# Kernel tuning notes

Measured on AMD Instinct MI355X. Metric: run time of the kernel, lower is better.

## Reference

```python
import jax, jax.numpy as jnp
import numpy as np

RES = 32
HEADS = 16
EMB = 1024
DIM_HEAD = EMB // HEADS
BATCH = 8
N = RES * RES
SCALE = DIM_HEAD ** -0.5


def _make_bias_idxs():
    # replicate the LeViT-style |dx|,|dy| offset indexing from __init__
    points = [(i, j) for i in range(RES) for j in range(RES)]
    offsets = {}
    idxs = []
    for p1 in points:
        for p2 in points:
            off = (abs(p1[0] - p2[0]), abs(p1[1] - p2[1]))
            if off not in offsets:
                offsets[off] = len(offsets)
            idxs.append(offsets[off])
    return np.asarray(idxs, dtype=np.int32).reshape(N, N), len(offsets)


def setup_inputs() -> dict:
    key = jax.random.key(0)
    k_x, k_qkv, k_b, k_o = jax.random.split(key, 4)
    bias_idxs, n_off = _make_bias_idxs()  # n_off == 1024 for a 32x32 grid
    return {
        "x": jax.random.normal(k_x, (BATCH, N, EMB), dtype=jnp.float32),
        "W_qkv": jax.random.normal(k_qkv, (3 * EMB, EMB), dtype=jnp.float32) * 0.02,
        "attention_biases": jax.random.normal(k_b, (HEADS, n_off), dtype=jnp.float32) * 0.02,
        "bias_idxs": jnp.asarray(bias_idxs),
        "W_out": jax.random.normal(k_o, (EMB, EMB), dtype=jnp.float32) * 0.02,
        "b_out": jnp.zeros((EMB,), dtype=jnp.float32),
    }


def reference(x, W_qkv, attention_biases, bias_idxs, W_out, b_out):
    B, n, E = x.shape
    # to_qkv: Linear(E, 3E, bias=False) -> x @ W^T
    qkv = x @ W_qkv.T  # [B, n, 3E]
    q, k, v = jnp.split(qkv, 3, axis=-1)

    def heads(t):  # b n (h d) -> b h n d
        return t.reshape(B, n, HEADS, DIM_HEAD).transpose(0, 2, 1, 3)

    q, k, v = heads(q), heads(k), heads(v)
    qk = jnp.einsum("bhnd,bhmd->bhnm", q, k) * SCALE  # [B, h, n, n]
    bias = attention_biases[:, bias_idxs]  # gather -> [h, n, n]
    qk = qk + bias[None]
    attn = jax.nn.softmax(qk, axis=-1)
    out = jnp.einsum("bhnm,bhmd->bhnd", attn, v)
    out = out.transpose(0, 2, 1, 3).reshape(B, n, E)  # b h n d -> b n (h d)
    # to_out: Linear(E, E) with bias (dropout p=0 is identity)
    return out @ W_out.T + b_out
```

## Files before the change

### kernel.cpp

```cpp
#include <hip/hip_runtime.h>

typedef __attribute__((ext_vector_type(8))) short bf16x8;
typedef __attribute__((ext_vector_type(4))) short bf16x4;
typedef __attribute__((ext_vector_type(4))) float f32x4;

#define L2E 1.44269504088896340736f
#define QSCL 0.18033688011112042f

__device__ inline unsigned short f2bf(float f) {
  union { float f; unsigned int u; } x; x.f = f;
  return (unsigned short)((x.u + 0x8000u) >> 16);
}
__device__ inline unsigned int f2bf2(float a, float b) {
  union { float f; unsigned int u; } xa, xb;
  xa.f = a; xb.f = b;
  return ((xa.u + 0x8000u) >> 16) | (((xb.u + 0x8000u) & 0xFFFF0000u));
}

__device__ inline void gl_lds16(const void* g, void* l) {
  __builtin_amdgcn_global_load_lds((const __attribute__((address_space(1))) void*)g,
                                   (__attribute__((address_space(3))) void*)l,
                                   16, 0, 0);
}

__global__ void cast_bf16_kernel(const float* __restrict__ in,
                                 unsigned short* __restrict__ out, int n4) {
  int i = blockIdx.x * blockDim.x + threadIdx.x;
  int st = gridDim.x * blockDim.x;
  for (; i < n4; i += st) {
    float4 v = reinterpret_cast<const float4*>(in)[i];
    ushort4 o;
    o.x = f2bf(v.x); o.y = f2bf(v.y); o.z = f2bf(v.z); o.w = f2bf(v.w);
    reinterpret_cast<ushort4*>(out)[i] = o;
  }
}

__global__ __launch_bounds__(256, 2) void gemm_qkv(
    const unsigned short* __restrict__ A,
    const unsigned short* __restrict__ Bm,
    unsigned short* __restrict__ qo,
    unsigned short* __restrict__ ko,
    unsigned short* __restrict__ vo) {
  __shared__ unsigned short sA[2][128 * 32];
  __shared__ unsigned short sB[2][128 * 32];
  __shared__ unsigned short sT[128 * 136];
  const int K = 1024;
  const int tid = threadIdx.x;
  const int w = tid >> 6, lane = tid & 63;
  const int l15 = lane & 15, quad = lane >> 4;
  const int wm = (w >> 1) * 64, wn = (w & 1) * 64;
  const int tm = blockIdx.y, tn = blockIdx.x;

  const unsigned short* Ab = A + (size_t)(tm * 128) * K;
  const unsigned short* Bb = Bm + (size_t)(tn * 128) * K;

  const int srow = w * 32 + (lane >> 2);
  const int scol = (lane & 3) * 8;

  const f32x4 fz = {0.f, 0.f, 0.f, 0.f};
  f32x4 acc[4][4];
#pragma unroll
  for (int i = 0; i < 4; i++)
#pragma unroll
    for (int j = 0; j < 4; j++) acc[i][j] = fz;

  gl_lds16(Ab + (size_t)srow * K + scol,        &sA[0][(w * 32) * 32]);
  gl_lds16(Ab + (size_t)(srow + 16) * K + scol, &sA[0][(w * 32 + 16) * 32]);
  gl_lds16(Bb + (size_t)srow * K + scol,        &sB[0][(w * 32) * 32]);
  gl_lds16(Bb + (size_t)(srow + 16) * K + scol, &sB[0][(w * 32 + 16) * 32]);

  int buf = 0;
  for (int k0 = 0; k0 < K; k0 += 32) {
    __syncthreads();
    if (k0 + 32 < K) {
      int nb = buf ^ 1, kn = k0 + 32;
      gl_lds16(Ab + (size_t)srow * K + kn + scol,        &sA[nb][(w * 32) * 32]);
      gl_lds16(Ab + (size_t)(srow + 16) * K + kn + scol, &sA[nb][(w * 32 + 16) * 32]);
      gl_lds16(Bb + (size_t)srow * K + kn + scol,        &sB[nb][(w * 32) * 32]);
      gl_lds16(Bb + (size_t)(srow + 16) * K + kn + scol, &sB[nb][(w * 32 + 16) * 32]);
    }
    bf16x8 af[4], bfr[4];
#pragma unroll
    for (int mt = 0; mt < 4; mt++) af[mt]  = *(const bf16x8*)&sA[buf][(wm + mt * 16 + l15) * 32 + quad * 8];
#pragma unroll
    for (int nt = 0; nt < 4; nt++) bfr[nt] = *(const bf16x8*)&sB[buf][(wn + nt * 16 + l15) * 32 + quad * 8];
#pragma unroll
    for (int mt = 0; mt < 4; mt++)
#pragma unroll
      for (int nt = 0; nt < 4; nt++)
        acc[mt][nt] = __builtin_amdgcn_mfma_f32_16x16x32_bf16(af[mt], bfr[nt], acc[mt][nt], 0, 0, 0);
    buf ^= 1;
  }

  const int c0 = tn * 128;
  const int which = c0 >> 10;
  const int m0 = tm * 128;
  const int bb = m0 >> 10, n0 = m0 & 1023;
  __syncthreads();
  if (which < 2) {
    const float scl = (which == 0) ? QSCL : 1.0f;
#pragma unroll
    for (int mt = 0; mt < 4; mt++)
#pragma unroll
      for (int nt = 0; nt < 4; nt++)
#pragma unroll
        for (int r = 0; r < 4; r++)
          sT[(wm + mt * 16 + quad * 4 + r) * 136 + wn + nt * 16 + l15] = f2bf(acc[mt][nt][r] * scl);
    __syncthreads();
    unsigned short* dst = (which == 0) ? qo : ko;
#pragma unroll
    for (int i = 0; i < 8; i++) {
      int u = tid + i * 256;
      int row = u >> 4, g = u & 15;
      int cg = c0 + g * 8;
      int hh = (cg & 1023) >> 6, d0 = cg & 63;
      uint4 val = *(const uint4*)&sT[row * 136 + g * 8];
      *(uint4*)&dst[(((size_t)bb * 16 + hh) * 1024 + n0 + row) * 64 + d0] = val;
    }
  } else {
#pragma unroll
    for (int mt = 0; mt < 4; mt++)
#pragma unroll
      for (int nt = 0; nt < 4; nt++)
#pragma unroll
        for (int r = 0; r < 4; r++)
          sT[(wn + nt * 16 + l15) * 136 + wm + mt * 16 + quad * 4 + r] = f2bf(acc[mt][nt][r]);
    __syncthreads();
#pragma unroll
    for (int i = 0; i < 8; i++) {
      int u = tid + i * 256;
      int col = u >> 4, g = u & 15;
      int cg = c0 + col;
      int hh = (cg & 1023) >> 6, dd = cg & 63;
      uint4 val = *(const uint4*)&sT[col * 136 + g * 8];
      *(uint4*)&vo[(((size_t)bb * 16 + hh) * 64 + dd) * 1024 + n0 + g * 8] = val;
    }
  }
}

__global__ __launch_bounds__(256, 4) void attn_kernel(
    const unsigned short* __restrict__ Q,
    const unsigned short* __restrict__ Kg,
    const unsigned short* __restrict__ Vt,
    const float* __restrict__ biases,
    unsigned short* __restrict__ Og) {
  __shared__ unsigned short sK[2][64 * 64];
  __shared__ unsigned short sV[2][64 * 64];
  __shared__ float sBias[1024];

  const int bx = blockIdx.x;
  const int bh = bx & 127, qt = bx >> 7;
  const int h = bh & 15, b = bh >> 4;
  const int tid = threadIdx.x, w = tid >> 6, lane = tid & 63;
  const int l15 = lane & 15, quad = lane >> 4;

  const size_t bhs = (size_t)(b * 16 + h);
  const unsigned short* qbase = Q + (bhs * 1024 + (size_t)qt * 128) * 64;
  const unsigned short* kbase = Kg + bhs * 1024 * 64;
  const unsigned short* vbase = Vt + bhs * 64 * 1024;

  for (int t = tid; t < 1024; t += 256) sBias[t] = biases[h * 1024 + t] * L2E;

  const int sr0 = w * 16 + (lane >> 3);
  const int sc8 = lane & 7;
  const int sw0 = sc8 ^ (lane >> 3);

  gl_lds16(kbase + (size_t)sr0 * 64 + sw0 * 8,        &sK[0][(w * 16) * 64]);
  gl_lds16(kbase + (size_t)(sr0 + 8) * 64 + sw0 * 8,  &sK[0][(w * 16 + 8) * 64]);
  gl_lds16(vbase + (size_t)sr0 * 1024 + sw0 * 8,      &sV[0][(w * 16) * 64]);
  gl_lds16(vbase + (size_t)(sr0 + 8) * 1024 + sw0 * 8,&sV[0][(w * 16 + 8) * 64]);

  bf16x8 qf[2][2];
#pragma unroll
  for (int qb = 0; qb < 2; qb++)
#pragma unroll
    for (int kd = 0; kd < 2; kd++)
      qf[qb][kd] = *(const bf16x8*)(qbase + (w * 32 + qb * 16 + l15) * 64 + kd * 32 + quad * 8);

  const int qg0 = qt * 128 + w * 32;
  int qi[2], qj[2];
#pragma unroll
  for (int qb = 0; qb < 2; qb++) {
    int qr = qg0 + qb * 16 + l15;
    qi[qb] = qr >> 5; qj[qb] = qr & 31;
  }
  const int kvq = quad * 4;

  float rsum[2] = {0.f, 0.f};
  const f32x4 fz = {0.f, 0.f, 0.f, 0.f};
  f32x4 of[2][4];
#pragma unroll
  for (int i = 0; i < 2; i++)
#pragma unroll
    for (int j = 0; j < 4; j++) of[i][j] = fz;

  int buf = 0;
  for (int j0 = 0; j0 < 1024; j0 += 64) {
    __syncthreads();
    if (j0 + 64 < 1024) {
      int nb = buf ^ 1, jn = j0 + 64;
      gl_lds16(kbase + (size_t)(jn + sr0) * 64 + sw0 * 8,       &sK[nb][(w * 16) * 64]);
      gl_lds16(kbase + (size_t)(jn + sr0 + 8) * 64 + sw0 * 8,   &sK[nb][(w * 16 + 8) * 64]);
      gl_lds16(vbase + (size_t)sr0 * 1024 + jn + sw0 * 8,       &sV[nb][(w * 16) * 64]);
      gl_lds16(vbase + (size_t)(sr0 + 8) * 1024 + jn + sw0 * 8, &sV[nb][(w * 16 + 8) * 64]);
    }
    const unsigned short* K_ = sK[buf];
    const unsigned short* V_ = sV[buf];
    const int j5 = j0 >> 5;

#pragma unroll
    for (int kvb = 0; kvb < 4; kvb++) {
      bf16x8 kf0 = *(const bf16x8*)&K_[(kvb * 16 + l15) * 64 + ((quad ^ (l15 & 7)) << 3)];
      bf16x8 kf1 = *(const bf16x8*)&K_[(kvb * 16 + l15) * 64 + (((4 + quad) ^ (l15 & 7)) << 3)];
      bf16x4 vf[4];
#pragma unroll
      for (int nt = 0; nt < 4; nt++) {
        int d = nt * 16 + l15;
        vf[nt] = *(const bf16x4*)&V_[d * 64 + (((kvb * 2 + (quad >> 1)) ^ (l15 & 7)) << 3) + (quad & 1) * 4];
      }
      const int kvi = j5 + (kvb >> 1);
      const int kvjb = (kvb & 1) * 16 + kvq;
#pragma unroll
      for (int qb = 0; qb < 2; qb++) {
        f32x4 s4 = __builtin_amdgcn_mfma_f32_16x16x32_bf16(kf0, qf[qb][0], fz, 0, 0, 0);
        s4 = __builtin_amdgcn_mfma_f32_16x16x32_bf16(kf1, qf[qb][1], s4, 0, 0, 0);
        const float* bb = sBias + (abs(qi[qb] - kvi) << 5);
        float p0 = __builtin_amdgcn_exp2f(s4.x + bb[abs(qj[qb] - kvjb)]);
        float p1 = __builtin_amdgcn_exp2f(s4.y + bb[abs(qj[qb] - (kvjb + 1))]);
        float p2 = __builtin_amdgcn_exp2f(s4.z + bb[abs(qj[qb] - (kvjb + 2))]);
        float p3 = __builtin_amdgcn_exp2f(s4.w + bb[abs(qj[qb] - (kvjb + 3))]);
        rsum[qb] += (p0 + p1) + (p2 + p3);
        union { unsigned int u[2]; bf16x4 v; } pk;
        pk.u[0] = f2bf2(p0, p1);
        pk.u[1] = f2bf2(p2, p3);
#pragma unroll
        for (int nt = 0; nt < 4; nt++)
          of[qb][nt] = __builtin_amdgcn_mfma_f32_16x16x16bf16_1k(pk.v, vf[nt], of[qb][nt], 0, 0, 0);
      }
    }
    buf ^= 1;
  }

#pragma unroll
  for (int qb = 0; qb < 2; qb++) {
    rsum[qb] += __shfl_xor(rsum[qb], 16);
    rsum[qb] += __shfl_xor(rsum[qb], 32);
  }

#pragma unroll
  for (int qb = 0; qb < 2; qb++)
#pragma unroll
    for (int r = 0; r < 4; r++) {
      float rv = __shfl(rsum[qb], kvq + r, 16);
      float inv = __builtin_amdgcn_rcpf(rv);
      int n = qg0 + qb * 16 + kvq + r;
      size_t orow = ((size_t)b * 1024 + n) * 1024 + h * 64;
#pragma unroll
      for (int nt = 0; nt < 4; nt++)
        Og[orow + nt * 16 + l15] = f2bf(of[qb][nt][r] * inv);
    }
}

__global__ __launch_bounds__(256, 2) void gemm_out_k(
    const unsigned short* __restrict__ A,
    const unsigned short* __restrict__ Bm,
    const float* __restrict__ bias,
    float* __restrict__ out) {
  __shared__ unsigned short sA[2][128 * 32];
  __shared__ unsigned short sB[2][128 * 32];
  const int K = 1024;
  const int tid = threadIdx.x;
  const int w = tid >> 6, lane = tid & 63;
  const int l15 = lane & 15, quad = lane >> 4;
  const int wm = (w >> 1) * 64, wn = (w & 1) * 64;
  const int tm = blockIdx.y, tn = blockIdx.x;

  const unsigned short* Ab = A + (size_t)(tm * 128) * K;
  const unsigned short* Bb = Bm + (size_t)(tn * 128) * K;

  const int srow = w * 32 + (lane >> 2);
  const int scol = (lane & 3) * 8;

  const f32x4 fz = {0.f, 0.f, 0.f, 0.f};
  f32x4 acc[4][4];
#pragma unroll
  for (int i = 0; i < 4; i++)
#pragma unroll
    for (int j = 0; j < 4; j++) acc[i][j] = fz;

  gl_lds16(Ab + (size_t)srow * K + scol,        &sA[0][(w * 32) * 32]);
  gl_lds16(Ab + (size_t)(srow + 16) * K + scol, &sA[0][(w * 32 + 16) * 32]);
  gl_lds16(Bb + (size_t)srow * K + scol,        &sB[0][(w * 32) * 32]);
  gl_lds16(Bb + (size_t)(srow + 16) * K + scol, &sB[0][(w * 32 + 16) * 32]);

  int buf = 0;
  for (int k0 = 0; k0 < K; k0 += 32) {
    __syncthreads();
    if (k0 + 32 < K) {
      int nb = buf ^ 1, kn = k0 + 32;
      gl_lds16(Ab + (size_t)srow * K + kn + scol,        &sA[nb][(w * 32) * 32]);
      gl_lds16(Ab + (size_t)(srow + 16) * K + kn + scol, &sA[nb][(w * 32 + 16) * 32]);
      gl_lds16(Bb + (size_t)srow * K + kn + scol,        &sB[nb][(w * 32) * 32]);
      gl_lds16(Bb + (size_t)(srow + 16) * K + kn + scol, &sB[nb][(w * 32 + 16) * 32]);
    }
    bf16x8 af[4], bfr[4];
#pragma unroll
    for (int mt = 0; mt < 4; mt++) af[mt]  = *(const bf16x8*)&sA[buf][(wm + mt * 16 + l15) * 32 + quad * 8];
#pragma unroll
    for (int nt = 0; nt < 4; nt++) bfr[nt] = *(const bf16x8*)&sB[buf][(wn + nt * 16 + l15) * 32 + quad * 8];
#pragma unroll
    for (int mt = 0; mt < 4; mt++)
#pragma unroll
      for (int nt = 0; nt < 4; nt++)
        acc[mt][nt] = __builtin_amdgcn_mfma_f32_16x16x32_bf16(af[mt], bfr[nt], acc[mt][nt], 0, 0, 0);
    buf ^= 1;
  }

  const int m0 = tm * 128 + wm, c0 = tn * 128 + wn;
#pragma unroll
  for (int mt = 0; mt < 4; mt++)
#pragma unroll
    for (int nt = 0; nt < 4; nt++)
#pragma unroll
      for (int r = 0; r < 4; r++) {
        int m = m0 + mt * 16 + quad * 4 + r;
        int c = c0 + nt * 16 + l15;
        out[(size_t)m * 1024 + c] = acc[mt][nt][r] + bias[c];
      }
}

extern "C" void kernel_launch(void* const* d_in, const int* in_sizes, int n_in,
                              void* d_out, int out_size, void* d_ws, size_t ws_size,
                              hipStream_t stream) {
  const float* x    = (const float*)d_in[0];
  const float* Wqkv = (const float*)d_in[1];
  const float* ab   = (const float*)d_in[2];
  const float* Wout = (const float*)d_in[4];
  const float* bout = (const float*)d_in[5];
  float* out = (float*)d_out;

  char* ws = (char*)d_ws;
  unsigned short* xb  = (unsigned short*)(ws);
  unsigned short* wqb = (unsigned short*)(ws + 16777216);
  unsigned short* wob = (unsigned short*)(ws + 23068672);
  unsigned short* qw  = (unsigned short*)(ws + 25165824);
  unsigned short* kw  = (unsigned short*)(ws + 41943040);
  unsigned short* vw  = (unsigned short*)(ws + 58720256);
  unsigned short* ow  = (unsigned short*)(ws + 75497472);

  cast_bf16_kernel<<<1024, 256, 0, stream>>>(x, xb, 8192 * 1024 / 4);
  cast_bf16_kernel<<<512, 256, 0, stream>>>(Wqkv, wqb, 3072 * 1024 / 4);
  cast_bf16_kernel<<<256, 256, 0, stream>>>(Wout, wob, 1024 * 1024 / 4);
  gemm_qkv<<<dim3(24, 64), 256, 0, stream>>>(xb, wqb, qw, kw, vw);
  attn_kernel<<<1024, 256, 0, stream>>>(qw, kw, vw, ab, ow);
  gemm_out_k<<<dim3(8, 64), 256, 0, stream>>>(ow, wob, bout, out);
}
```

Baseline: 264.9 us.

## Swizzle GEMM LDS tiles, drop epilogue staging, split QKV GEMM by output mode

Applies an XOR swizzle to the LDS layout of the A/B tiles in both GEMMs to reduce bank conflicts. The QKV GEMM epilogue no longer stages through a shared transpose buffer. Operand order in the MFMA is swapped for Q/K, and V is written directly, so each lane stores 8-byte packed bf16 values. The QKV GEMM is split into two template launches (Q/K and V), and launch bounds are raised to 4 blocks per SM for more occupancy. Explicit vmcnt(0) waits are added before the barriers so async global->LDS loads have landed. The risk is narrower uncoalesced stores and a second kernel launch.

```diff
diff --git a/kernel.cpp b/kernel.cpp
--- a/kernel.cpp
+++ b/kernel.cpp
@@ -21,6 +21,10 @@
   __builtin_amdgcn_global_load_lds((const __attribute__((address_space(1))) void*)g,
                                    (__attribute__((address_space(3))) void*)l,
                                    16, 0, 0);
+}
+
+__device__ inline void vm_drain() {
+  asm volatile("s_waitcnt vmcnt(0)" ::: "memory");
 }
 
 __global__ void cast_bf16_kernel(const float* __restrict__ in,
@@ -35,7 +39,8 @@
   }
 }
 
-__global__ __launch_bounds__(256, 2) void gemm_qkv(
+template <int MODE>
+__global__ __launch_bounds__(256, 4) void gemm_qkv_t(
     const unsigned short* __restrict__ A,
     const unsigned short* __restrict__ Bm,
     unsigned short* __restrict__ qo,
@@ -43,19 +48,20 @@
     unsigned short* __restrict__ vo) {
   __shared__ unsigned short sA[2][128 * 32];
   __shared__ unsigned short sB[2][128 * 32];
-  __shared__ unsigned short sT[128 * 136];
   const int K = 1024;
   const int tid = threadIdx.x;
   const int w = tid >> 6, lane = tid & 63;
   const int l15 = lane & 15, quad = lane >> 4;
   const int wm = (w >> 1) * 64, wn = (w & 1) * 64;
-  const int tm = blockIdx.y, tn = blockIdx.x;
+  const int tm = blockIdx.y;
+  const int tn = (MODE == 0) ? blockIdx.x : blockIdx.x + 16;
 
   const unsigned short* Ab = A + (size_t)(tm * 128) * K;
   const unsigned short* Bb = Bm + (size_t)(tn * 128) * K;
 
   const int srow = w * 32 + (lane >> 2);
-  const int scol = (lane & 3) * 8;
+  const int scol = (((lane & 3) ^ ((lane >> 3) & 3))) * 8;
+  const int rsw = (l15 >> 1) & 3;
 
   const f32x4 fz = {0.f, 0.f, 0.f, 0.f};
   f32x4 acc[4][4];
@@ -71,6 +77,7 @@
 
   int buf = 0;
   for (int k0 = 0; k0 < K; k0 += 32) {
+    vm_drain();
     __syncthreads();
     if (k0 + 32 < K) {
       int nb = buf ^ 1, kn = k0 + 32;
@@ -81,59 +88,57 @@
     }
     bf16x8 af[4], bfr[4];
 #pragma unroll
-    for (int mt = 0; mt < 4; mt++) af[mt]  = *(const bf16x8*)&sA[buf][(wm + mt * 16 + l15) * 32 + quad * 8];
-#pragma unroll
-    for (int nt = 0; nt < 4; nt++) bfr[nt] = *(const bf16x8*)&sB[buf][(wn + nt * 16 + l15) * 32 + quad * 8];
-#pragma unroll
     for (int mt = 0; mt < 4; mt++)
-#pragma unroll
-      for (int nt = 0; nt < 4; nt++)
-        acc[mt][nt] = __builtin_amdgcn_mfma_f32_16x16x32_bf16(af[mt], bfr[nt], acc[mt][nt], 0, 0, 0);
+      af[mt] = *(const bf16x8*)&sA[buf][(wm + mt * 16 + l15) * 32 + ((quad ^ rsw) << 3)];
+#pragma unroll
+    for (int nt = 0; nt < 4; nt++)
+      bfr[nt] = *(const bf16x8*)&sB[buf][(wn + nt * 16 + l15) * 32 + ((quad ^ rsw) << 3)];
+#pragma unroll
+    for (int mt = 0; mt < 4; mt++)
+#pragma unroll
+      for (int nt = 0; nt < 4; nt++) {
+        if (MODE == 0)
+          acc[mt][nt] = __builtin_amdgcn_mfma_f32_16x16x32_bf16(bfr[nt], af[mt], acc[mt][nt], 0, 0, 0);
+        else
+          acc[mt][nt] = __builtin_amdgcn_mfma_f32_16x16x32_bf16(af[mt], bfr[nt], acc[mt][nt], 0, 0, 0);
+      }
     buf ^= 1;
   }
 
-  const int c0 = tn * 128;
-  const int which = c0 >> 10;
   const int m0 = tm * 128;
   const int bb = m0 >> 10, n0 = m0 & 1023;
-  __syncthreads();
-  if (which < 2) {
+  const int cbase = (tn * 128) & 1023;
+
+  if (MODE == 0) {
+    const int which = tn >> 3;
     const float scl = (which == 0) ? QSCL : 1.0f;
-#pragma unroll
-    for (int mt = 0; mt < 4; mt++)
-#pragma unroll
-      for (int nt = 0; nt < 4; nt++)
-#pragma unroll
-        for (int r = 0; r < 4; r++)
-          sT[(wm + mt * 16 + quad * 4 + r) * 136 + wn + nt * 16 + l15] = f2bf(acc[mt][nt][r] * scl);
-    __syncthreads();
     unsigned short* dst = (which == 0) ? qo : ko;
 #pragma unroll
-    for (int i = 0; i < 8; i++) {
-      int u = tid + i * 256;
-      int row = u >> 4, g = u & 15;
-      int cg = c0 + g * 8;
-      int hh = (cg & 1023) >> 6, d0 = cg & 63;
-      uint4 val = *(const uint4*)&sT[row * 136 + g * 8];
-      *(uint4*)&dst[(((size_t)bb * 16 + hh) * 1024 + n0 + row) * 64 + d0] = val;
+    for (int mt = 0; mt < 4; mt++) {
+      int tok = n0 + wm + mt * 16 + l15;
+#pragma unroll
+      for (int nt = 0; nt < 4; nt++) {
+        int c = cbase + wn + nt * 16 + quad * 4;
+        int hh = c >> 6, d0 = c & 63;
+        uint2 val;
+        val.x = f2bf2(acc[mt][nt][0] * scl, acc[mt][nt][1] * scl);
+        val.y = f2bf2(acc[mt][nt][2] * scl, acc[mt][nt][3] * scl);
+        *(uint2*)&dst[(((size_t)bb * 16 + hh) * 1024 + tok) * 64 + d0] = val;
+      }
     }
   } else {
 #pragma unroll
-    for (int mt = 0; mt < 4; mt++)
-#pragma unroll
-      for (int nt = 0; nt < 4; nt++)
-#pragma unroll
-        for (int r = 0; r < 4; r++)
-          sT[(wn + nt * 16 + l15) * 136 + wm + mt * 16 + quad * 4 + r] = f2bf(acc[mt][nt][r]);
-    __syncthreads();
-#pragma unroll
-    for (int i = 0; i < 8; i++) {
-      int u = tid + i * 256;
-      int col = u >> 4, g = u & 15;
-      int cg = c0 + col;
-      int hh = (cg & 1023) >> 6, dd = cg & 63;
-      uint4 val = *(const uint4*)&sT[col * 136 + g * 8];
-      *(uint4*)&vo[(((size_t)bb * 16 + hh) * 64 + dd) * 1024 + n0 + g * 8] = val;
+    for (int mt = 0; mt < 4; mt++) {
+      int tok = n0 + wm + mt * 16 + quad * 4;
+#pragma unroll
+      for (int nt = 0; nt < 4; nt++) {
+        int c = cbase + wn + nt * 16 + l15;
+        int hh = c >> 6, dd = c & 63;
+        uint2 val;
+        val.x = f2bf2(acc[mt][nt][0], acc[mt][nt][1]);
+        val.y = f2bf2(acc[mt][nt][2], acc[mt][nt][3]);
+        *(uint2*)&vo[(((size_t)bb * 16 + hh) * 64 + dd) * 1024 + tok] = val;
+      }
     }
   }
 }
@@ -196,6 +201,7 @@
 
   int buf = 0;
   for (int j0 = 0; j0 < 1024; j0 += 64) {
+    vm_drain();
     __syncthreads();
     if (j0 + 64 < 1024) {
       int nb = buf ^ 1, jn = j0 + 64;
@@ -261,7 +267,7 @@
     }
 }
 
-__global__ __launch_bounds__(256, 2) void gemm_out_k(
+__global__ __launch_bounds__(256, 4) void gemm_out_k(
     const unsigned short* __restrict__ A,
     const unsigned short* __restrict__ Bm,
     const float* __restrict__ bias,
@@ -279,7 +285,8 @@
   const unsigned short* Bb = Bm + (size_t)(tn * 128) * K;
 
   const int srow = w * 32 + (lane >> 2);
-  const int scol = (lane & 3) * 8;
+  const int scol = (((lane & 3) ^ ((lane >> 3) & 3))) * 8;
+  const int rsw = (l15 >> 1) & 3;
 
   const f32x4 fz = {0.f, 0.f, 0.f, 0.f};
   f32x4 acc[4][4];
@@ -295,6 +302,7 @@
 
   int buf = 0;
   for (int k0 = 0; k0 < K; k0 += 32) {
+    vm_drain();
     __syncthreads();
     if (k0 + 32 < K) {
       int nb = buf ^ 1, kn = k0 + 32;
@@ -305,9 +313,11 @@
     }
     bf16x8 af[4], bfr[4];
 #pragma unroll
-    for (int mt = 0; mt < 4; mt++) af[mt]  = *(const bf16x8*)&sA[buf][(wm + mt * 16 + l15) * 32 + quad * 8];
-#pragma unroll
-    for (int nt = 0; nt < 4; nt++) bfr[nt] = *(const bf16x8*)&sB[buf][(wn + nt * 16 + l15) * 32 + quad * 8];
+    for (int mt = 0; mt < 4; mt++)
+      af[mt] = *(const bf16x8*)&sA[buf][(wm + mt * 16 + l15) * 32 + ((quad ^ rsw) << 3)];
+#pragma unroll
+    for (int nt = 0; nt < 4; nt++)
+      bfr[nt] = *(const bf16x8*)&sB[buf][(wn + nt * 16 + l15) * 32 + ((quad ^ rsw) << 3)];
 #pragma unroll
     for (int mt = 0; mt < 4; mt++)
 #pragma unroll
@@ -351,7 +361,8 @@
   cast_bf16_kernel<<<1024, 256, 0, stream>>>(x, xb, 8192 * 1024 / 4);
   cast_bf16_kernel<<<512, 256, 0, stream>>>(Wqkv, wqb, 3072 * 1024 / 4);
   cast_bf16_kernel<<<256, 256, 0, stream>>>(Wout, wob, 1024 * 1024 / 4);
-  gemm_qkv<<<dim3(24, 64), 256, 0, stream>>>(xb, wqb, qw, kw, vw);
+  gemm_qkv_t<0><<<dim3(16, 64), 256, 0, stream>>>(xb, wqb, qw, kw, vw);
+  gemm_qkv_t<1><<<dim3(8, 64), 256, 0, stream>>>(xb, wqb, qw, kw, vw);
   attn_kernel<<<1024, 256, 0, stream>>>(qw, kw, vw, ab, ow);
   gemm_out_k<<<dim3(8, 64), 256, 0, stream>>>(ow, wob, bout, out);
 }
```

After: 274.6 us. 1.04x slower.
